# Kernel optimization log

Measured on AMD Instinct MI355X. Metric: run time of the kernel, lower is better.

Reference implementation:

```python
import jax, jax.numpy as jnp
import numpy as np

B, N, M = 32, 4096, 128
PRESENCE_W = 1.0
L1_W = 1.0


def setup_inputs() -> dict:
    key = jax.random.key(0)
    k1, k2, k3 = jax.random.split(key, 3)
    return {
        "predict_scores": jax.random.normal(k1, (B, N, 2), jnp.float32),
        "predict_points": jax.random.uniform(k2, (B, N, 2), dtype=jnp.float32),
        "scores": jnp.ones((B, M), jnp.int32),  # class label 1 == object present
        "points": jax.random.uniform(k3, (B, M, 2), dtype=jnp.float32),
    }


def _cost_matrix(predict_scores, predict_points, scores, points):
    # probs: [B, N, 2]
    probs = jax.nn.softmax(predict_scores, axis=-1)
    Bc, Nc, _ = probs.shape
    Mc = scores.shape[1]
    # presence cost: -probs[b, i, scores[b, j]] -> [B, N, M]
    idx = jnp.broadcast_to(scores[:, None, :], (Bc, Nc, Mc))
    presence = -jnp.take_along_axis(probs, idx, axis=2)
    # L1 cdist: [B, N, M]
    l1 = jnp.sum(jnp.abs(predict_points[:, :, None, :] - points[:, None, :, :]), axis=-1)
    return PRESENCE_W * presence + L1_W * l1


def _lsa(cost):
    """Pure-numpy linear_sum_assignment (Jonker-Volgenant shortest augmenting
    path, same algorithm as scipy). cost: [R, C] float64. Returns (row_ind,
    col_ind) sorted by row index, matching scipy semantics."""
    transpose = cost.shape[1] < cost.shape[0]
    Cm = cost.T if transpose else cost
    n, m = Cm.shape  # n <= m
    u = np.zeros(n)
    v = np.zeros(m)
    path = np.full(m, -1, dtype=np.int64)
    col4row = np.full(n, -1, dtype=np.int64)
    row4col = np.full(m, -1, dtype=np.int64)
    for cur_row in range(n):
        shortest = np.full(m, np.inf)
        SR = np.zeros(n, dtype=bool)
        SC = np.zeros(m, dtype=bool)
        min_val = 0.0
        i = cur_row
        sink = -1
        while sink == -1:
            SR[i] = True
            idxs = np.nonzero(~SC)[0]
            r = min_val + Cm[i, idxs] - u[i] - v[idxs]
            better = r < shortest[idxs]
            upd = idxs[better]
            path[upd] = i
            shortest[upd] = r[better]
            j = idxs[np.argmin(shortest[idxs])]
            min_val = shortest[j]
            if row4col[j] == -1:
                sink = j
            else:
                i = row4col[j]
            SC[j] = True
        # update dual variables
        u[cur_row] += min_val
        other = SR.copy()
        other[cur_row] = False
        if other.any():
            u[other] += min_val - shortest[col4row[other]]
        v[SC] -= min_val - shortest[SC]
        # augment along alternating path
        j = sink
        while True:
            i = path[j]
            row4col[j] = i
            col4row[i], j = j, col4row[i]
            if i == cur_row:
                break
    if transpose:
        order = np.argsort(col4row)
        return col4row[order], order
    return np.arange(n), col4row


def reference(predict_scores, predict_points, scores, points):
    cost = _cost_matrix(predict_scores, predict_points, scores, points)
    cost_np = np.asarray(jax.device_get(cost), dtype=np.float64)
    batch_all, rows_all, cols_all = [], [], []
    for b in range(cost_np.shape[0]):
        r, c = _lsa(cost_np[b])
        batch_all.append(np.full(r.shape, b, dtype=np.int64))
        rows_all.append(r.astype(np.int64))
        cols_all.append(c.astype(np.int64))
    batch_idx = jnp.asarray(np.concatenate(batch_all))
    src_idx = jnp.asarray(np.concatenate(rows_all))
    tgt_idx = jnp.asarray(np.concatenate(cols_all))
    return (batch_idx, src_idx, tgt_idx)
```

## Files before the change

kernel.cpp:

```cpp
#include <hip/hip_runtime.h>


#define Bb 32
#define Nn 4096
#define Mm 128
#define Tt 512
#define Kk (Nn / Tt)
#define TSH 9
#define NW (Tt / 64)
#define RECMAX 160

#define DPP_CMB(CTRL, RMASK)                                                   \
    {                                                                          \
        int tlo = __builtin_amdgcn_update_dpp(0,          rlo, CTRL, RMASK, 0xF, false); \
        int thi = __builtin_amdgcn_update_dpp(0x7FF00000, rhi, CTRL, RMASK, 0xF, false); \
        int tmm = __builtin_amdgcn_update_dpp(0x7FFFFFFF, rmm, CTRL, RMASK, 0xF, false); \
        double tv = __hiloint2double(thi, tlo);                                \
        double cv = __hiloint2double(rhi, rlo);                                \
        bool tk = (tv < cv) || (tv == cv && tmm < rmm);                        \
        rlo = tk ? tlo : rlo; rhi = tk ? thi : rhi; rmm = tk ? tmm : rmm;      \
    }

__global__ __launch_bounds__(Tt, 1)
void hungarian_kernel(const float* __restrict__ predict_scores,
                      const float* __restrict__ predict_points,
                      const int*   __restrict__ scores,
                      const float* __restrict__ points,
                      int* __restrict__ out)
{
    __shared__ double vvl[Nn];
    __shared__ short  path_lds[Nn];
    __shared__ short  row4col[Nn];
    __shared__ double uu[Mm];
    __shared__ short  col4row[Mm];
    __shared__ double srow_val[Mm];
    __shared__ unsigned char SRr[Mm];
    __shared__ float  tx0[Mm], tx1[Mm];
    __shared__ int    tch[Mm];
    __shared__ short  scol[RECMAX];
    __shared__ double sval[RECMAX];
    __shared__ int    nsc_lds;
    __shared__ double wv_[2][NW];
    __shared__ int    wm_[2][NW];

    const int b    = blockIdx.x;
    const int tid  = threadIdx.x;
    const int lane = tid & 63;
    const int wid  = tid >> 6;
    const double INFD = __builtin_inf();
    const double NAND = __builtin_nan("");

    float negp0[Kk], negp1[Kk], qx0[Kk], qx1[Kk];
    const float* ps = predict_scores + (size_t)b * Nn * 2;
    const float* pp = predict_points + (size_t)b * Nn * 2;
    #pragma unroll
    for (int k = 0; k < Kk; ++k) {
        int j = tid + (k << TSH);
        float2 sc = ((const float2*)ps)[j];
        float mx = fmaxf(sc.x, sc.y);
        float e0 = expf(sc.x - mx), e1 = expf(sc.y - mx);
        float sm = e0 + e1;
        float n0 = -(e0 / sm), n1 = -(e1 / sm);
        float2 qp = ((const float2*)pp)[j];
        negp0[k] = n0; negp1[k] = n1;
        qx0[k] = qp.x; qx1[k] = qp.y;
        vvl[j] = 0.0;
        row4col[j] = -1;
    }
    if (tid < Mm) {
        col4row[tid] = -1;
        SRr[tid] = 0;
        uu[tid] = 0.0;
        tx0[tid] = points[(size_t)b * Mm * 2 + 2 * tid];
        tx1[tid] = points[(size_t)b * Mm * 2 + 2 * tid + 1];
        tch[tid] = scores[(size_t)b * Mm + tid];
    }
    __syncthreads();

    const float t0_c0 = tx0[lane], t0_c1 = tx0[lane + 64];
    const float t1_c0 = tx1[lane], t1_c1 = tx1[lane + 64];
    const int   ch_c0 = tch[lane], ch_c1 = tch[lane + 64];

    int pathv[Kk];
    #pragma unroll
    for (int k = 0; k < Kk; ++k) pathv[k] = 0;

    #define RELAX(PRES)                                                        \
        _Pragma("unroll")                                                      \
        for (int k = 0; k < Kk; ++k) {                                         \
            float cf = PRES[k] + (fabsf(qx0[k] - it0) + fabsf(qx1[k] - it1));  \
            double r = ((minv + (double)cf) - ui) - vreg[k];                   \
            bool upd = r < shr[k];                                             \
            shr[k] = upd ? r : shr[k];                                         \
            pathv[k] = upd ? i : pathv[k];                                     \
            double sj = shr[k];                                                \
            if (sj < bv) { bv = sj; bm = premeta[k]; }                         \
        }

    for (int cur_row = 0; cur_row < Mm; ++cur_row) {
        double shr[Kk], vreg[Kk];
        int    premeta[Kk];
        double u_c0 = uu[lane], u_c1 = uu[lane + 64];
        #pragma unroll
        for (int k = 0; k < Kk; ++k) {
            int j = tid + (k << TSH);
            shr[k]  = INFD;
            vreg[k] = vvl[j];
            premeta[k] = (j << 8) | ((int)row4col[j] + 1);
        }
        int    i = cur_row;
        double minv = 0.0;
        int    sink = -1, par = 0, nsc = 0;
        double ui  = uu[cur_row];
        float  it0 = tx0[cur_row], it1 = tx1[cur_row];
        int    ich = __builtin_amdgcn_readfirstlane((tch[cur_row] == 1) ? 1 : 0);

        for (;;) {
            double bv = INFD; int bm = 0x7FFFFFFF;
            if (ich) { RELAX(negp1) } else { RELAX(negp0) }

            int rlo = __double2loint(bv), rhi = __double2hiint(bv), rmm = bm;
            DPP_CMB(0x121, 0xF)
            DPP_CMB(0x122, 0xF)
            DPP_CMB(0x124, 0xF)
            DPP_CMB(0x128, 0xF)
            DPP_CMB(0x142, 0xA)
            DPP_CMB(0x143, 0xC)
            if (lane == 63) {
                wv_[par][wid] = __hiloint2double(rhi, rlo);
                wm_[par][wid] = rmm;
            }
            __syncthreads();

            {
                int l8 = lane & 7;
                double cv8 = wv_[par][l8];
                rlo = __double2loint(cv8); rhi = __double2hiint(cv8);
                rmm = wm_[par][l8];
            }
            DPP_CMB(0x121, 0xF)
            DPP_CMB(0x122, 0xF)
            DPP_CMB(0x124, 0xF)
            par ^= 1;
            int mm_s = __builtin_amdgcn_readfirstlane(rmm);
            minv = __hiloint2double(__builtin_amdgcn_readfirstlane(rhi),
                                    __builtin_amdgcn_readfirstlane(rlo));
            int bj = mm_s >> 8;
            int r4 = (mm_s & 0xFF) - 1;
            if (r4 < 0) {
                if (tid == 0) nsc_lds = nsc;
                sink = bj;
                break;
            }
            {
                const bool me = (tid == (bj & (Tt - 1)));
                switch (bj >> TSH) {
                    case 0: if (me) shr[0] = NAND; break;
                    case 1: if (me) shr[1] = NAND; break;
                    case 2: if (me) shr[2] = NAND; break;
                    case 3: if (me) shr[3] = NAND; break;
                    case 4: if (me) shr[4] = NAND; break;
                    case 5: if (me) shr[5] = NAND; break;
                    case 6: if (me) shr[6] = NAND; break;
                    default: if (me) shr[7] = NAND; break;
                }
            }
            if (tid == 0) {
                SRr[r4] = 1; srow_val[r4] = minv;
                scol[nsc] = (short)bj; sval[nsc] = minv; ++nsc;
            }
            i = r4;
            {
                int  lx = r4 & 63;
                bool hi = r4 >= 64;
                double us = hi ? u_c1 : u_c0;
                float  f0 = hi ? t0_c1 : t0_c0;
                float  f1 = hi ? t1_c1 : t1_c0;
                int    cs = hi ? ch_c1 : ch_c0;
                ui  = __hiloint2double(
                        __builtin_amdgcn_readlane(__double2hiint(us), lx),
                        __builtin_amdgcn_readlane(__double2loint(us), lx));
                it0 = __int_as_float(
                        __builtin_amdgcn_readlane(__float_as_int(f0), lx));
                it1 = __int_as_float(
                        __builtin_amdgcn_readlane(__float_as_int(f1), lx));
                ich = (__builtin_amdgcn_readlane(cs, lx) == 1) ? 1 : 0;
            }
        }

        #pragma unroll
        for (int k = 0; k < Kk; ++k)
            path_lds[tid + (k << TSH)] = (short)pathv[k];
        __syncthreads();

        const double minvF = minv;
        if (tid < Mm) {
            if (tid == cur_row)   uu[tid] += minvF;
            else if (SRr[tid])    uu[tid] += minvF - srow_val[tid];
            SRr[tid] = 0;
        }
        int S = nsc_lds;
        if (tid < S) {
            int jc = scol[tid];
            vvl[jc] -= (minvF - sval[tid]);
        }
        if (tid == 0) {
            int j = sink;
            for (;;) {
                int i2 = path_lds[j];
                row4col[j] = (short)i2;
                int nxt = col4row[i2];
                col4row[i2] = (short)j;
                j = nxt;
                if (i2 == cur_row) break;
            }
        }
        __syncthreads();
    }
    #undef RELAX

    if (tid < Mm) {
        int myj = col4row[tid];
        int rank = 0;
        #pragma unroll 4
        for (int t = 0; t < Mm; ++t) rank += (col4row[t] < myj) ? 1 : 0;
        out[b * Mm + tid] = b;
        out[Bb * Mm + b * Mm + rank] = myj;
        out[2 * Bb * Mm + b * Mm + rank] = tid;
    }
}

extern "C" void kernel_launch(void* const* d_in, const int* in_sizes, int n_in,
                              void* d_out, int out_size, void* d_ws, size_t ws_size,
                              hipStream_t stream) {
    (void)in_sizes; (void)n_in; (void)d_ws; (void)ws_size; (void)out_size;
    const float* predict_scores = (const float*)d_in[0];
    const float* predict_points = (const float*)d_in[1];
    const int*   scores         = (const int*)d_in[2];
    const float* points         = (const float*)d_in[3];
    int* out = (int*)d_out;
    hipLaunchKernelGGL(hungarian_kernel, dim3(Bb), dim3(Tt), 0, stream,
                       predict_scores, predict_points, scores, points, out);
}
```

Measured before the change: 510.8 us.

## Split argmin reduction into value-min then index-min and prepack augment path

The per-thread running argmin inside the relax loop is replaced by a tree fmin over the eight slots followed by an index pick. The lexicographic DPP reduction becomes a cheaper double fmin pass followed by an integer min pass over matching candidates. The serial augmentation walk now reads a packed word holding both the path row and that row's prior column, which removes one dependent LDS load per step. The packing is only valid if col4row entries along the path are not changed before they are read; augmentation writes each row once, so this should hold, but it adds gathers of col4row for every column each row.

After: 484.8 us. -5.1%, faster.

```diff
diff --git a/kernel.cpp b/kernel.cpp
--- a/kernel.cpp
+++ b/kernel.cpp
@@ -9,16 +9,31 @@
 #define TSH 9
 #define NW (Tt / 64)
 #define RECMAX 160
-
-#define DPP_CMB(CTRL, RMASK)                                                   \
+#define IMAX 0x7FFFFFFF
+
+#define DPP_VFMIN(CTRL)                                                        \
     {                                                                          \
-        int tlo = __builtin_amdgcn_update_dpp(0,          rlo, CTRL, RMASK, 0xF, false); \
-        int thi = __builtin_amdgcn_update_dpp(0x7FF00000, rhi, CTRL, RMASK, 0xF, false); \
-        int tmm = __builtin_amdgcn_update_dpp(0x7FFFFFFF, rmm, CTRL, RMASK, 0xF, false); \
+        int tlo = __builtin_amdgcn_update_dpp(0,          vlo, CTRL, 0xF, 0xF, false); \
+        int thi = __builtin_amdgcn_update_dpp(0x7FF00000, vhi, CTRL, 0xF, 0xF, false); \
         double tv = __hiloint2double(thi, tlo);                                \
-        double cv = __hiloint2double(rhi, rlo);                                \
-        bool tk = (tv < cv) || (tv == cv && tmm < rmm);                        \
-        rlo = tk ? tlo : rlo; rhi = tk ? thi : rhi; rmm = tk ? tmm : rmm;      \
+        double cv0 = __hiloint2double(vhi, vlo);                               \
+        double nv = fmin(cv0, tv);                                             \
+        vlo = __double2loint(nv); vhi = __double2hiint(nv);                    \
+    }
+#define DPP_IMIN(CTRL)                                                         \
+    {                                                                          \
+        int tm = __builtin_amdgcn_update_dpp(IMAX, vmm, CTRL, 0xF, 0xF, false); \
+        vmm = min(vmm, tm);                                                    \
+    }
+#define DPP_LEX(CTRL, RMASK)                                                   \
+    {                                                                          \
+        int tlo = __builtin_amdgcn_update_dpp(0,          vlo, CTRL, RMASK, 0xF, false); \
+        int thi = __builtin_amdgcn_update_dpp(0x7FF00000, vhi, CTRL, RMASK, 0xF, false); \
+        int tmm = __builtin_amdgcn_update_dpp(IMAX,       vmm, CTRL, RMASK, 0xF, false); \
+        double tv = __hiloint2double(thi, tlo);                                \
+        double cv0 = __hiloint2double(vhi, vlo);                               \
+        bool tk = (tv < cv0) || (tv == cv0 && tmm < vmm);                      \
+        vlo = tk ? tlo : vlo; vhi = tk ? thi : vhi; vmm = tk ? tmm : vmm;      \
     }
 
 __global__ __launch_bounds__(Tt, 1)
@@ -29,7 +44,7 @@
                       int* __restrict__ out)
 {
     __shared__ double vvl[Nn];
-    __shared__ short  path_lds[Nn];
+    __shared__ int    path_pack[Nn];
     __shared__ short  row4col[Nn];
     __shared__ double uu[Mm];
     __shared__ short  col4row[Mm];
@@ -40,8 +55,7 @@
     __shared__ short  scol[RECMAX];
     __shared__ double sval[RECMAX];
     __shared__ int    nsc_lds;
-    __shared__ double wv_[2][NW];
-    __shared__ int    wm_[2][NW];
+    __shared__ int4   wcand[2][NW];
 
     const int b    = blockIdx.x;
     const int tid  = threadIdx.x;
@@ -93,8 +107,6 @@
             bool upd = r < shr[k];                                             \
             shr[k] = upd ? r : shr[k];                                         \
             pathv[k] = upd ? i : pathv[k];                                     \
-            double sj = shr[k];                                                \
-            if (sj < bv) { bv = sj; bm = premeta[k]; }                         \
         }
 
     for (int cur_row = 0; cur_row < Mm; ++cur_row) {
@@ -116,35 +128,46 @@
         int    ich = __builtin_amdgcn_readfirstlane((tch[cur_row] == 1) ? 1 : 0);
 
         for (;;) {
-            double bv = INFD; int bm = 0x7FFFFFFF;
             if (ich) { RELAX(negp1) } else { RELAX(negp0) }
 
-            int rlo = __double2loint(bv), rhi = __double2hiint(bv), rmm = bm;
-            DPP_CMB(0x121, 0xF)
-            DPP_CMB(0x122, 0xF)
-            DPP_CMB(0x124, 0xF)
-            DPP_CMB(0x128, 0xF)
-            DPP_CMB(0x142, 0xA)
-            DPP_CMB(0x143, 0xC)
-            if (lane == 63) {
-                wv_[par][wid] = __hiloint2double(rhi, rlo);
-                wm_[par][wid] = rmm;
-            }
+            double a0 = fmin(shr[0], shr[1]), a1 = fmin(shr[2], shr[3]);
+            double a2 = fmin(shr[4], shr[5]), a3 = fmin(shr[6], shr[7]);
+            double bv = fmin(fmin(fmin(a0, a1), fmin(a2, a3)), INFD);
+            int c0 = (shr[0] == bv) ? premeta[0] : IMAX;
+            int c1 = (shr[1] == bv) ? premeta[1] : IMAX;
+            int c2 = (shr[2] == bv) ? premeta[2] : IMAX;
+            int c3 = (shr[3] == bv) ? premeta[3] : IMAX;
+            int c4 = (shr[4] == bv) ? premeta[4] : IMAX;
+            int c5 = (shr[5] == bv) ? premeta[5] : IMAX;
+            int c6 = (shr[6] == bv) ? premeta[6] : IMAX;
+            int c7 = (shr[7] == bv) ? premeta[7] : IMAX;
+            int bm = min(min(min(c0, c1), min(c2, c3)),
+                         min(min(c4, c5), min(c6, c7)));
+
+            int vlo = __double2loint(bv), vhi = __double2hiint(bv), vmm;
+            DPP_VFMIN(0x121) DPP_VFMIN(0x122) DPP_VFMIN(0x124) DPP_VFMIN(0x128)
+            {
+                double rv = __hiloint2double(vhi, vlo);
+                vmm = (bv == rv) ? bm : IMAX;
+            }
+            DPP_IMIN(0x121) DPP_IMIN(0x122) DPP_IMIN(0x124) DPP_IMIN(0x128)
+            DPP_LEX(0x142, 0xA)
+            DPP_LEX(0x143, 0xC)
+            if (lane == 63) wcand[par][wid] = make_int4(vlo, vhi, vmm, 0);
             __syncthreads();
 
-            {
-                int l8 = lane & 7;
-                double cv8 = wv_[par][l8];
-                rlo = __double2loint(cv8); rhi = __double2hiint(cv8);
-                rmm = wm_[par][l8];
-            }
-            DPP_CMB(0x121, 0xF)
-            DPP_CMB(0x122, 0xF)
-            DPP_CMB(0x124, 0xF)
+            int4 cnd = wcand[par][lane & 7];
+            double cv2 = __hiloint2double(cnd.y, cnd.x);
+            int    cm2 = cnd.z;
+            vlo = cnd.x; vhi = cnd.y;
+            DPP_VFMIN(0x121) DPP_VFMIN(0x122) DPP_VFMIN(0x124)
+            double gv = __hiloint2double(vhi, vlo);
+            vmm = (cv2 == gv) ? cm2 : IMAX;
+            DPP_IMIN(0x121) DPP_IMIN(0x122) DPP_IMIN(0x124)
             par ^= 1;
-            int mm_s = __builtin_amdgcn_readfirstlane(rmm);
-            minv = __hiloint2double(__builtin_amdgcn_readfirstlane(rhi),
-                                    __builtin_amdgcn_readfirstlane(rlo));
+            minv = __hiloint2double(__builtin_amdgcn_readfirstlane(vhi),
+                                    __builtin_amdgcn_readfirstlane(vlo));
+            int mm_s = __builtin_amdgcn_readfirstlane(vmm);
             int bj = mm_s >> 8;
             int r4 = (mm_s & 0xFF) - 1;
             if (r4 < 0) {
@@ -189,8 +212,11 @@
         }
 
         #pragma unroll
-        for (int k = 0; k < Kk; ++k)
-            path_lds[tid + (k << TSH)] = (short)pathv[k];
+        for (int k = 0; k < Kk; ++k) {
+            int pv = pathv[k];
+            int cr = (int)(unsigned short)col4row[pv];
+            path_pack[tid + (k << TSH)] = (pv & 0xFFFF) | (cr << 16);
+        }
         __syncthreads();
 
         const double minvF = minv;
@@ -207,12 +233,12 @@
         if (tid == 0) {
             int j = sink;
             for (;;) {
-                int i2 = path_lds[j];
+                int pk = path_pack[j];
+                int i2 = pk & 0xFFFF;
                 row4col[j] = (short)i2;
-                int nxt = col4row[i2];
                 col4row[i2] = (short)j;
-                j = nxt;
                 if (i2 == cur_row) break;
+                j = (pk >> 16) & 0xFFFF;
             }
         }
         __syncthreads();
```
